# Kernel optimization log

Measured on AMD Instinct MI355X. Metric: run time of the kernel, lower is better.

## Reference

```python
import jax, jax.numpy as jnp
import numpy as np

B, S, D = 4, 4096, 768


def setup_inputs() -> dict:
    key = jax.random.key(0)
    kx, kk, kv, kq = jax.random.split(key, 4)
    scale = 1.0 / np.sqrt(D)
    x = jax.random.normal(kx, (B, S, D), dtype=jnp.float32)
    Wk = jax.random.normal(kk, (D, D), dtype=jnp.float32) * scale
    Wv = jax.random.normal(kv, (D, D), dtype=jnp.float32) * scale
    Wq = jax.random.normal(kq, (D, D), dtype=jnp.float32) * scale
    # nn.Parameter(torch.zeros(1)) -> use small nonzero so output depends on hrr path
    gain = jnp.full((1,), 0.1, dtype=jnp.float32)
    return {"x": x, "Wk": Wk, "Wv": Wv, "Wq": Wq, "gain": gain}


def reference(x, Wk, Wv, Wq, gain):
    # Linear projections (torch Linear: y = x @ W.T)
    k = jnp.einsum('bsd,ed->bse', x, Wk)
    v = jnp.einsum('bsd,ed->bse', x, Wv)
    q = jnp.einsum('bsd,ed->bse', x, Wq)
    d = x.shape[-1]
    # HRR binding: circular convolution in Fourier domain
    kf = jnp.fft.rfft(k, axis=-1)          # [B,S,D//2+1] complex
    vf = jnp.fft.rfft(v, axis=-1)
    qf = jnp.fft.rfft(q, axis=-1)
    # causal cumulative memory of bound key-value pairs
    mem = jnp.cumsum(kf * vf, axis=1)
    # unbind with query via circular correlation (approx inverse = conj)
    values_hat = jnp.fft.irfft(mem * jnp.conj(qf), n=d, axis=-1)
    return x + values_hat * gain
```

## Files before the change

### kernel.cpp

```cpp
#include <hip/hip_runtime.h>
#include <math.h>

#define D_DIM 768
#define NF    385
#define NSP   772
#define BATCH 4
#define SEQ   4096
#define MROWS 16384
#define KP5   800
#define SPECZ ((size_t)NSP * MROWS)

typedef __bf16 bf16x8 __attribute__((ext_vector_type(8)));
typedef float  f32x4  __attribute__((ext_vector_type(4)));

__device__ __forceinline__ void gl2lds16(const __bf16* g, __bf16* l) {
    __builtin_amdgcn_global_load_lds(
        (const __attribute__((address_space(1))) void*)g,
        (__attribute__((address_space(3))) void*)l, 16, 0, 0);
}

__global__ void build_tables(__bf16* __restrict__ FtabT, __bf16* __restrict__ GT) {
    int idx = blockIdx.x * blockDim.x + threadIdx.x;
    int stride = gridDim.x * blockDim.x;
    const float w0 = 6.28318530717958647692f / (float)D_DIM;
    for (int i = idx; i < NF * D_DIM; i += stride) {
        int f = i / D_DIM, e = i - f * D_DIM;
        int m = (e * f) % D_DIM;
        float s, c;
        __sincosf(w0 * (float)m, &s, &c);
        FtabT[(size_t)(2*f)   * D_DIM + e] = (__bf16)c;
        FtabT[(size_t)(2*f+1) * D_DIM + e] = (__bf16)(-s);
        bool dcny = (f == 0) || (f == NF - 1);
        float w = dcny ? (1.0f / D_DIM) : (2.0f / D_DIM);
        GT[(size_t)e * KP5 + 2*f]     = (__bf16)(w * c);
        GT[(size_t)e * KP5 + 2*f + 1] = dcny ? (__bf16)0.0f : (__bf16)(-w * s);
    }
    for (int i = idx; i < 2 * D_DIM; i += stride)
        FtabT[(size_t)770 * D_DIM + i] = (__bf16)0.0f;
    for (int i = idx; i < D_DIM * (KP5 - 2 * NF); i += stride) {
        int r = i / (KP5 - 2 * NF), c = 2 * NF + (i % (KP5 - 2 * NF));
        GT[(size_t)r * KP5 + c] = (__bf16)0.0f;
    }
}

__global__ void cvt_x(const float* __restrict__ xin, __bf16* __restrict__ xout) {
    int idx = blockIdx.x * blockDim.x + threadIdx.x;
    int stride = gridDim.x * blockDim.x;
    const int total8 = MROWS * D_DIM / 8;
    const float4* x4 = (const float4*)xin;
    for (int i = idx; i < total8; i += stride) {
        float4 a = x4[2*i], b = x4[2*i+1];
        bf16x8 o;
        o[0]=(__bf16)a.x; o[1]=(__bf16)a.y; o[2]=(__bf16)a.z; o[3]=(__bf16)a.w;
        o[4]=(__bf16)b.x; o[5]=(__bf16)b.y; o[6]=(__bf16)b.z; o[7]=(__bf16)b.w;
        *((bf16x8*)xout + i) = o;
    }
}

__global__ void transposeW(const float* __restrict__ W0, const float* __restrict__ W1,
                           const float* __restrict__ W2, __bf16* __restrict__ WT) {
    const float* W = blockIdx.z == 0 ? W0 : (blockIdx.z == 1 ? W1 : W2);
    __shared__ float tile[32][33];
    const int tx = threadIdx.x, ty = threadIdx.y;
    const int e0 = blockIdx.x * 32, d0 = blockIdx.y * 32;
    #pragma unroll
    for (int j = 0; j < 4; ++j)
        tile[ty + j*8][tx] = W[(size_t)(e0 + ty + j*8) * D_DIM + d0 + tx];
    __syncthreads();
    __bf16* WTz = WT + (size_t)blockIdx.z * D_DIM * D_DIM;
    #pragma unroll
    for (int j = 0; j < 4; ++j)
        WTz[(size_t)(d0 + ty + j*8) * D_DIM + e0 + tx] = (__bf16)tile[tx][ty + j*8];
}

__global__ void transposeO(const __bf16* __restrict__ OT, __bf16* __restrict__ O) {
    __shared__ __bf16 tile[32][34];
    const int tx = threadIdx.x, ty = threadIdx.y;
    const int m0 = blockIdx.x * 32, c0 = blockIdx.y * 32;
    #pragma unroll
    for (int j = 0; j < 4; ++j) {
        int c = c0 + ty + j*8;
        __bf16 v = (__bf16)0.0f;
        if (c < NSP) v = OT[(size_t)c * MROWS + m0 + tx];
        tile[ty + j*8][tx] = v;
    }
    __syncthreads();
    #pragma unroll
    for (int j = 0; j < 4; ++j)
        O[(size_t)(m0 + ty + j*8) * KP5 + c0 + tx] = tile[tx][ty + j*8];
}

__global__ __launch_bounds__(256) void mfma_nt(
    const __bf16* __restrict__ A, const __bf16* __restrict__ B, void* __restrict__ Cv,
    int M, int N, int K, int lda, int ldb, int ldc,
    long strideAz, long strideCz, int c_bf16,
    const float* __restrict__ addend, const float* __restrict__ gain)
{
    __shared__ __bf16 As[128 * 32];
    __shared__ __bf16 Bs[128 * 32];
    const int tid  = threadIdx.x;
    const int wave = tid >> 6, lane = tid & 63;
    const int lrow = lane & 15, lquad = lane >> 4;
    const int wm = wave >> 1, wn = wave & 1;
    const int m0 = blockIdx.y * 128, n0 = blockIdx.x * 128;
    const __bf16* Az = A + (size_t)blockIdx.z * strideAz;

    const int sr = tid >> 2;
    const int sc = (((tid & 3) ^ ((tid >> 3) & 3))) * 8;
    int ra0 = m0 + sr;      if (ra0 > M - 1) ra0 = M - 1;
    int ra1 = m0 + sr + 64; if (ra1 > M - 1) ra1 = M - 1;
    const int rb0 = n0 + sr, rb1 = n0 + sr + 64;
    __bf16* ldsA0 = As + wave * 512;
    __bf16* ldsA1 = As + 2048 + wave * 512;
    __bf16* ldsB0 = Bs + wave * 512;
    __bf16* ldsB1 = Bs + 2048 + wave * 512;

    const int swz = (lrow >> 1) & 3;
    const int fragcol = (lquad ^ swz) * 8;

    f32x4 acc[4][4];
    #pragma unroll
    for (int i = 0; i < 4; ++i)
        #pragma unroll
        for (int j = 0; j < 4; ++j)
            acc[i][j] = (f32x4){0.f, 0.f, 0.f, 0.f};

    for (int k0 = 0; k0 < K; k0 += 32) {
        gl2lds16(Az + (size_t)ra0 * lda + k0 + sc, ldsA0);
        gl2lds16(Az + (size_t)ra1 * lda + k0 + sc, ldsA1);
        gl2lds16(B  + (size_t)rb0 * ldb + k0 + sc, ldsB0);
        gl2lds16(B  + (size_t)rb1 * ldb + k0 + sc, ldsB1);
        __syncthreads();
        bf16x8 af[4], bfr[4];
        #pragma unroll
        for (int i = 0; i < 4; ++i) {
            af[i]  = *(const bf16x8*)&As[(wm*64 + i*16 + lrow) * 32 + fragcol];
            bfr[i] = *(const bf16x8*)&Bs[(wn*64 + i*16 + lrow) * 32 + fragcol];
        }
        #pragma unroll
        for (int i = 0; i < 4; ++i)
            #pragma unroll
            for (int j = 0; j < 4; ++j)
                acc[i][j] = __builtin_amdgcn_mfma_f32_16x16x32_bf16(
                    af[i], bfr[j], acc[i][j], 0, 0, 0);
        __syncthreads();
    }

    const int colb = n0 + wn * 64 + lrow;
    const int rowb = m0 + wm * 64 + lquad * 4;
    if (c_bf16) {
        __bf16* C = (__bf16*)Cv + (size_t)blockIdx.z * strideCz;
        #pragma unroll
        for (int i = 0; i < 4; ++i)
            #pragma unroll
            for (int j = 0; j < 4; ++j) {
                const int col = colb + j * 16;
                #pragma unroll
                for (int r = 0; r < 4; ++r) {
                    const int mm = rowb + i * 16 + r;
                    if (mm < M) C[(size_t)mm * ldc + col] = (__bf16)acc[i][j][r];
                }
            }
    } else if (addend) {
        float* C = (float*)Cv;
        const float g = gain[0];
        #pragma unroll
        for (int i = 0; i < 4; ++i)
            #pragma unroll
            for (int j = 0; j < 4; ++j) {
                const int col = colb + j * 16;
                #pragma unroll
                for (int r = 0; r < 4; ++r) {
                    const int mm = rowb + i * 16 + r;
                    if (mm < M) {
                        const size_t off = (size_t)mm * ldc + col;
                        C[off] = addend[off] + g * acc[i][j][r];
                    }
                }
            }
    } else {
        float* C = (float*)Cv + (size_t)blockIdx.z * strideCz;
        #pragma unroll
        for (int i = 0; i < 4; ++i)
            #pragma unroll
            for (int j = 0; j < 4; ++j) {
                const int col = colb + j * 16;
                #pragma unroll
                for (int r = 0; r < 4; ++r) {
                    const int mm = rowb + i * 16 + r;
                    if (mm < M) C[(size_t)mm * ldc + col] = acc[i][j][r];
                }
            }
    }
}

__global__ __launch_bounds__(256) void scan_blocks(__bf16* __restrict__ spec) {
    const int blk = blockIdx.x;
    const int b = blk / NF, f = blk % NF;
    const int tid = threadIdx.x;
    const int lane = tid & 63, wid = tid >> 6;
    const size_t colbase = (size_t)b * SEQ;
    __bf16* Kre = spec + (size_t)(2*f) * MROWS + colbase;
    __bf16* Kim = Kre + MROWS;
    const __bf16* Vre = Kre + SPECZ;
    const __bf16* Vim = Vre + MROWS;
    const __bf16* Qre = Kre + 2 * SPECZ;
    const __bf16* Qim = Qre + MROWS;
    const int s0 = tid * 16;

    bf16x8 kr0 = *(const bf16x8*)(Kre + s0), kr1 = *(const bf16x8*)(Kre + s0 + 8);
    bf16x8 ki0 = *(const bf16x8*)(Kim + s0), ki1 = *(const bf16x8*)(Kim + s0 + 8);
    bf16x8 vr0 = *(const bf16x8*)(Vre + s0), vr1 = *(const bf16x8*)(Vre + s0 + 8);
    bf16x8 vi0 = *(const bf16x8*)(Vim + s0), vi1 = *(const bf16x8*)(Vim + s0 + 8);

    float pr[16], pi[16];
    #pragma unroll
    for (int u = 0; u < 8; ++u) {
        float a = (float)kr0[u], bq = (float)ki0[u], c = (float)vr0[u], d = (float)vi0[u];
        pr[u] = a * c - bq * d;
        pi[u] = a * d + bq * c;
        float a1 = (float)kr1[u], b1 = (float)ki1[u], c1 = (float)vr1[u], d1 = (float)vi1[u];
        pr[8+u] = a1 * c1 - b1 * d1;
        pi[8+u] = a1 * d1 + b1 * c1;
    }
    #pragma unroll
    for (int j = 1; j < 16; ++j) { pr[j] += pr[j-1]; pi[j] += pi[j-1]; }
    const float totr = pr[15], toti = pi[15];

    float sr = totr, si = toti;
    #pragma unroll
    for (int d = 1; d < 64; d <<= 1) {
        float ur = __shfl_up(sr, d, 64);
        float ui = __shfl_up(si, d, 64);
        if (lane >= d) { sr += ur; si += ui; }
    }
    __shared__ float wsr[4], wsi[4];
    if (lane == 63) { wsr[wid] = sr; wsi[wid] = si; }
    __syncthreads();
    float baser = 0.f, basei = 0.f;
    #pragma unroll
    for (int w = 0; w < 3; ++w)
        if (w < wid) { baser += wsr[w]; basei += wsi[w]; }
    const float exr = baser + sr - totr;
    const float exi = basei + si - toti;

    bf16x8 qr0 = *(const bf16x8*)(Qre + s0), qr1 = *(const bf16x8*)(Qre + s0 + 8);
    bf16x8 qi0 = *(const bf16x8*)(Qim + s0), qi1 = *(const bf16x8*)(Qim + s0 + 8);
    bf16x8 outr0, outr1, outi0, outi1;
    #pragma unroll
    for (int u = 0; u < 8; ++u) {
        float mr = exr + pr[u],   mi = exi + pi[u];
        float qr = (float)qr0[u], qi = (float)qi0[u];
        outr0[u] = (__bf16)(mr * qr + mi * qi);
        outi0[u] = (__bf16)(mi * qr - mr * qi);
        float mr1 = exr + pr[8+u], mi1 = exi + pi[8+u];
        float qr_ = (float)qr1[u], qi_ = (float)qi1[u];
        outr1[u] = (__bf16)(mr1 * qr_ + mi1 * qi_);
        outi1[u] = (__bf16)(mi1 * qr_ - mr1 * qi_);
    }
    *(bf16x8*)(Kre + s0)     = outr0;
    *(bf16x8*)(Kre + s0 + 8) = outr1;
    *(bf16x8*)(Kim + s0)     = outi0;
    *(bf16x8*)(Kim + s0 + 8) = outi1;
}

extern "C" void kernel_launch(void* const* d_in, const int* in_sizes, int n_in,
                              void* d_out, int out_size, void* d_ws, size_t ws_size,
                              hipStream_t stream) {
    const float* x    = (const float*)d_in[0];
    const float* Wk   = (const float*)d_in[1];
    const float* Wv   = (const float*)d_in[2];
    const float* Wq   = (const float*)d_in[3];
    const float* gain = (const float*)d_in[4];
    float* out = (float*)d_out;

    __bf16* FtabT = (__bf16*)d_ws;
    __bf16* GT    = FtabT + (size_t)NSP * D_DIM;
    __bf16* WT    = GT    + (size_t)D_DIM * KP5;
    __bf16* x16   = WT    + (size_t)3 * D_DIM * D_DIM;
    __bf16* CT    = x16   + (size_t)MROWS * D_DIM;
    __bf16* spec  = CT    + (size_t)NSP * 3 * D_DIM;
    __bf16* O     = spec  + SPECZ;

    build_tables<<<1184, 256, 0, stream>>>(FtabT, GT);
    cvt_x<<<3072, 256, 0, stream>>>(x, x16);
    transposeW<<<dim3(24, 24, 3), dim3(32, 8), 0, stream>>>(Wk, Wv, Wq, WT);

    mfma_nt<<<dim3(18, 7, 1), 256, 0, stream>>>(
        FtabT, WT, CT, NSP, 3 * D_DIM, D_DIM,
        D_DIM, D_DIM, 3 * D_DIM, 0, 0, 1, nullptr, nullptr);

    mfma_nt<<<dim3(128, 7, 3), 256, 0, stream>>>(
        CT, x16, spec, NSP, MROWS, D_DIM,
        3 * D_DIM, D_DIM, MROWS, (long)D_DIM, (long)SPECZ, 1, nullptr, nullptr);

    scan_blocks<<<BATCH * NF, 256, 0, stream>>>(spec);

    transposeO<<<dim3(512, 25), dim3(32, 8), 0, stream>>>(spec, O);

    mfma_nt<<<dim3(6, 128, 1), 256, 0, stream>>>(
        O, GT, out, MROWS, D_DIM, KP5,
        KP5, KP5, D_DIM, 0, 0, 0, x, gain);
}
```

Measured before the change: 308.2 us.

## Stack per-projection spectra, merge prologue kernels, and widen the output transpose

The three setup kernels (twiddle tables, x conversion to bf16, weight transpose) become one launch whose block ranges dispatch to each task. The Fourier-projected weights are stored as three stacked [NSP][D] slabs, so the large spectrum GEMM runs as one M=3*772 problem with 19 row tiles instead of 3×7 tiles, cutting padded MFMA work. The spectrum transpose now uses 64×64 tiles with 32-bit loads and stores that pack re/im pairs. The cost is extra stride parameters in the GEMM and more complex block-index logic in the fused prologue.

```diff
diff --git a/kernel.cpp b/kernel.cpp
--- a/kernel.cpp
+++ b/kernel.cpp
@@ -19,81 +19,98 @@
         (__attribute__((address_space(3))) void*)l, 16, 0, 0);
 }
 
-__global__ void build_tables(__bf16* __restrict__ FtabT, __bf16* __restrict__ GT) {
-    int idx = blockIdx.x * blockDim.x + threadIdx.x;
-    int stride = gridDim.x * blockDim.x;
-    const float w0 = 6.28318530717958647692f / (float)D_DIM;
-    for (int i = idx; i < NF * D_DIM; i += stride) {
-        int f = i / D_DIM, e = i - f * D_DIM;
-        int m = (e * f) % D_DIM;
-        float s, c;
-        __sincosf(w0 * (float)m, &s, &c);
-        FtabT[(size_t)(2*f)   * D_DIM + e] = (__bf16)c;
-        FtabT[(size_t)(2*f+1) * D_DIM + e] = (__bf16)(-s);
-        bool dcny = (f == 0) || (f == NF - 1);
-        float w = dcny ? (1.0f / D_DIM) : (2.0f / D_DIM);
-        GT[(size_t)e * KP5 + 2*f]     = (__bf16)(w * c);
-        GT[(size_t)e * KP5 + 2*f + 1] = dcny ? (__bf16)0.0f : (__bf16)(-w * s);
-    }
-    for (int i = idx; i < 2 * D_DIM; i += stride)
-        FtabT[(size_t)770 * D_DIM + i] = (__bf16)0.0f;
-    for (int i = idx; i < D_DIM * (KP5 - 2 * NF); i += stride) {
-        int r = i / (KP5 - 2 * NF), c = 2 * NF + (i % (KP5 - 2 * NF));
-        GT[(size_t)r * KP5 + c] = (__bf16)0.0f;
-    }
-}
-
-__global__ void cvt_x(const float* __restrict__ xin, __bf16* __restrict__ xout) {
-    int idx = blockIdx.x * blockDim.x + threadIdx.x;
-    int stride = gridDim.x * blockDim.x;
-    const int total8 = MROWS * D_DIM / 8;
-    const float4* x4 = (const float4*)xin;
-    for (int i = idx; i < total8; i += stride) {
-        float4 a = x4[2*i], b = x4[2*i+1];
-        bf16x8 o;
-        o[0]=(__bf16)a.x; o[1]=(__bf16)a.y; o[2]=(__bf16)a.z; o[3]=(__bf16)a.w;
-        o[4]=(__bf16)b.x; o[5]=(__bf16)b.y; o[6]=(__bf16)b.z; o[7]=(__bf16)b.w;
-        *((bf16x8*)xout + i) = o;
-    }
-}
-
-__global__ void transposeW(const float* __restrict__ W0, const float* __restrict__ W1,
-                           const float* __restrict__ W2, __bf16* __restrict__ WT) {
-    const float* W = blockIdx.z == 0 ? W0 : (blockIdx.z == 1 ? W1 : W2);
-    __shared__ float tile[32][33];
-    const int tx = threadIdx.x, ty = threadIdx.y;
-    const int e0 = blockIdx.x * 32, d0 = blockIdx.y * 32;
-    #pragma unroll
-    for (int j = 0; j < 4; ++j)
-        tile[ty + j*8][tx] = W[(size_t)(e0 + ty + j*8) * D_DIM + d0 + tx];
+__global__ __launch_bounds__(256) void prologue(
+    __bf16* __restrict__ FtabT, __bf16* __restrict__ GT,
+    const float* __restrict__ W0, const float* __restrict__ W1,
+    const float* __restrict__ W2, __bf16* __restrict__ WT,
+    const float* __restrict__ x, __bf16* __restrict__ x16)
+{
+    const int bid = blockIdx.x;
+    const int tid = threadIdx.x;
+    if (bid < 1728) {
+        __shared__ float tile[32][33];
+        const int bz = bid / 576, rem = bid % 576;
+        const int bx = rem % 24, by = rem / 24;
+        const float* W = bz == 0 ? W0 : (bz == 1 ? W1 : W2);
+        const int tx = tid & 31, ty = tid >> 5;
+        const int e0 = bx * 32, d0 = by * 32;
+        #pragma unroll
+        for (int j = 0; j < 4; ++j)
+            tile[ty + j*8][tx] = W[(size_t)(e0 + ty + j*8) * D_DIM + d0 + tx];
+        __syncthreads();
+        __bf16* WTz = WT + (size_t)bz * D_DIM * D_DIM;
+        #pragma unroll
+        for (int j = 0; j < 4; ++j)
+            WTz[(size_t)(d0 + ty + j*8) * D_DIM + e0 + tx] = (__bf16)tile[tx][ty + j*8];
+    } else if (bid < 2240) {
+        int idx = (bid - 1728) * 256 + tid;
+        const int stride = 512 * 256;
+        const float w0 = 6.28318530717958647692f / (float)D_DIM;
+        for (int i = idx; i < NF * D_DIM; i += stride) {
+            int f = i / D_DIM, e = i - f * D_DIM;
+            int m = (e * f) % D_DIM;
+            float s, c;
+            __sincosf(w0 * (float)m, &s, &c);
+            FtabT[(size_t)(2*f)   * D_DIM + e] = (__bf16)c;
+            FtabT[(size_t)(2*f+1) * D_DIM + e] = (__bf16)(-s);
+            bool dcny = (f == 0) || (f == NF - 1);
+            float w = dcny ? (1.0f / D_DIM) : (2.0f / D_DIM);
+            GT[(size_t)e * KP5 + 2*f]     = (__bf16)(w * c);
+            GT[(size_t)e * KP5 + 2*f + 1] = dcny ? (__bf16)0.0f : (__bf16)(-w * s);
+        }
+        for (int i = idx; i < 2 * D_DIM; i += stride)
+            FtabT[(size_t)770 * D_DIM + i] = (__bf16)0.0f;
+        for (int i = idx; i < D_DIM * (KP5 - 2 * NF); i += stride) {
+            int r = i / (KP5 - 2 * NF), c = 2 * NF + (i % (KP5 - 2 * NF));
+            GT[(size_t)r * KP5 + c] = (__bf16)0.0f;
+        }
+    } else {
+        int idx = (bid - 2240) * 256 + tid;
+        const int stride = 1024 * 256;
+        const int total8 = MROWS * D_DIM / 8;
+        const float4* x4 = (const float4*)x;
+        for (int i = idx; i < total8; i += stride) {
+            float4 a = x4[2*i], b = x4[2*i+1];
+            bf16x8 o;
+            o[0]=(__bf16)a.x; o[1]=(__bf16)a.y; o[2]=(__bf16)a.z; o[3]=(__bf16)a.w;
+            o[4]=(__bf16)b.x; o[5]=(__bf16)b.y; o[6]=(__bf16)b.z; o[7]=(__bf16)b.w;
+            *((bf16x8*)x16 + i) = o;
+        }
+    }
+}
+
+__global__ __launch_bounds__(256) void transposeO64(
+    const unsigned short* __restrict__ OT, unsigned short* __restrict__ O)
+{
+    __shared__ unsigned short tile[64][66];
+    const int tid = threadIdx.x;
+    const int m0 = blockIdx.x * 64, c0 = blockIdx.y * 64;
+    const int half = tid & 31, row8 = tid >> 5;
+    #pragma unroll
+    for (int p = 0; p < 8; ++p) {
+        const int c = c0 + p * 8 + row8;
+        unsigned int v = 0;
+        if (c < NSP)
+            v = *(const unsigned int*)(OT + (size_t)c * MROWS + m0 + half * 2);
+        *(unsigned int*)&tile[p * 8 + row8][half * 2] = v;
+    }
     __syncthreads();
-    __bf16* WTz = WT + (size_t)blockIdx.z * D_DIM * D_DIM;
-    #pragma unroll
-    for (int j = 0; j < 4; ++j)
-        WTz[(size_t)(d0 + ty + j*8) * D_DIM + e0 + tx] = (__bf16)tile[tx][ty + j*8];
-}
-
-__global__ void transposeO(const __bf16* __restrict__ OT, __bf16* __restrict__ O) {
-    __shared__ __bf16 tile[32][34];
-    const int tx = threadIdx.x, ty = threadIdx.y;
-    const int m0 = blockIdx.x * 32, c0 = blockIdx.y * 32;
-    #pragma unroll
-    for (int j = 0; j < 4; ++j) {
-        int c = c0 + ty + j*8;
-        __bf16 v = (__bf16)0.0f;
-        if (c < NSP) v = OT[(size_t)c * MROWS + m0 + tx];
-        tile[ty + j*8][tx] = v;
-    }
-    __syncthreads();
-    #pragma unroll
-    for (int j = 0; j < 4; ++j)
-        O[(size_t)(m0 + ty + j*8) * KP5 + c0 + tx] = tile[tx][ty + j*8];
+    #pragma unroll
+    for (int p = 0; p < 8; ++p) {
+        const int m = m0 + p * 8 + row8;
+        const int c = c0 + half * 2;
+        if (c < KP5) {
+            unsigned int re = tile[half * 2][p * 8 + row8];
+            unsigned int im = tile[half * 2 + 1][p * 8 + row8];
+            *(unsigned int*)(O + (size_t)m * KP5 + c) = (im << 16) | re;
+        }
+    }
 }
 
 __global__ __launch_bounds__(256) void mfma_nt(
     const __bf16* __restrict__ A, const __bf16* __restrict__ B, void* __restrict__ Cv,
     int M, int N, int K, int lda, int ldb, int ldc,
-    long strideAz, long strideCz, int c_bf16,
+    long strideAz, long strideBz, long strideCz, int c_bf16,
     const float* __restrict__ addend, const float* __restrict__ gain)
 {
     __shared__ __bf16 As[128 * 32];
@@ -104,6 +121,7 @@
     const int wm = wave >> 1, wn = wave & 1;
     const int m0 = blockIdx.y * 128, n0 = blockIdx.x * 128;
     const __bf16* Az = A + (size_t)blockIdx.z * strideAz;
+    const __bf16* Bz = B + (size_t)blockIdx.z * strideBz;
 
     const int sr = tid >> 2;
     const int sc = (((tid & 3) ^ ((tid >> 3) & 3))) * 8;
@@ -128,8 +146,8 @@
     for (int k0 = 0; k0 < K; k0 += 32) {
         gl2lds16(Az + (size_t)ra0 * lda + k0 + sc, ldsA0);
         gl2lds16(Az + (size_t)ra1 * lda + k0 + sc, ldsA1);
-        gl2lds16(B  + (size_t)rb0 * ldb + k0 + sc, ldsB0);
-        gl2lds16(B  + (size_t)rb1 * ldb + k0 + sc, ldsB1);
+        gl2lds16(Bz + (size_t)rb0 * ldb + k0 + sc, ldsB0);
+        gl2lds16(Bz + (size_t)rb1 * ldb + k0 + sc, ldsB1);
         __syncthreads();
         bf16x8 af[4], bfr[4];
         #pragma unroll
@@ -278,27 +296,27 @@
     __bf16* GT    = FtabT + (size_t)NSP * D_DIM;
     __bf16* WT    = GT    + (size_t)D_DIM * KP5;
     __bf16* x16   = WT    + (size_t)3 * D_DIM * D_DIM;
-    __bf16* CT    = x16   + (size_t)MROWS * D_DIM;
-    __bf16* spec  = CT    + (size_t)NSP * 3 * D_DIM;
+    __bf16* CTs   = x16   + (size_t)MROWS * D_DIM;
+    __bf16* spec  = CTs   + (size_t)3 * NSP * D_DIM;
     __bf16* O     = spec  + SPECZ;
 
-    build_tables<<<1184, 256, 0, stream>>>(FtabT, GT);
-    cvt_x<<<3072, 256, 0, stream>>>(x, x16);
-    transposeW<<<dim3(24, 24, 3), dim3(32, 8), 0, stream>>>(Wk, Wv, Wq, WT);
-
-    mfma_nt<<<dim3(18, 7, 1), 256, 0, stream>>>(
-        FtabT, WT, CT, NSP, 3 * D_DIM, D_DIM,
-        D_DIM, D_DIM, 3 * D_DIM, 0, 0, 1, nullptr, nullptr);
-
-    mfma_nt<<<dim3(128, 7, 3), 256, 0, stream>>>(
-        CT, x16, spec, NSP, MROWS, D_DIM,
-        3 * D_DIM, D_DIM, MROWS, (long)D_DIM, (long)SPECZ, 1, nullptr, nullptr);
+    prologue<<<3264, 256, 0, stream>>>(FtabT, GT, Wk, Wv, Wq, WT, x, x16);
+
+    mfma_nt<<<dim3(6, 7, 3), 256, 0, stream>>>(
+        FtabT, WT, CTs, NSP, D_DIM, D_DIM,
+        D_DIM, D_DIM, D_DIM,
+        0L, (long)D_DIM * D_DIM, (long)NSP * D_DIM, 1, nullptr, nullptr);
+
+    mfma_nt<<<dim3(128, 19, 1), 256, 0, stream>>>(
+        CTs, x16, spec, 3 * NSP, MROWS, D_DIM,
+        D_DIM, D_DIM, MROWS, 0L, 0L, 0L, 1, nullptr, nullptr);
 
     scan_blocks<<<BATCH * NF, 256, 0, stream>>>(spec);
 
-    transposeO<<<dim3(512, 25), dim3(32, 8), 0, stream>>>(spec, O);
+    transposeO64<<<dim3(MROWS / 64, 13), 256, 0, stream>>>(
+        (const unsigned short*)spec, (unsigned short*)O);
 
     mfma_nt<<<dim3(6, 128, 1), 256, 0, stream>>>(
         O, GT, out, MROWS, D_DIM, KP5,
-        KP5, KP5, D_DIM, 0, 0, 0, x, gain);
-}
+        KP5, KP5, D_DIM, 0L, 0L, 0L, 0, x, gain);
+}
```

Result: no change. 305.7 us (-0.8%).
